# Optimization experiments

Measured on AMD Instinct MI355X. Metric: run time of the kernel, lower is better.

## Reference

```python
import jax, jax.numpy as jnp
import numpy as np

PART_BODY = jnp.array([4, 4, 0, 0, 1, 1, 2, 2, 3, 3], dtype=jnp.int32)  # joint -> body part
NUM_SUBSET = 3
BN_EPS = 1e-5
NEG_SLOPE = 0.1


def setup_inputs() -> dict:
    key = jax.random.key(0)
    ks = jax.random.split(key, 8)
    N, C, T, V, S = 32, 96, 1024, 10, NUM_SUBSET
    P = 5  # number of body parts
    return {
        "x": jax.random.normal(ks[0], (N, C, T, V), dtype=jnp.float32),
        "b_att": jax.random.normal(ks[1], (N, S, P, P), dtype=jnp.float32),
        "W_qkv": jax.random.normal(ks[2], (3 * C, C), dtype=jnp.float32) * (1.0 / np.sqrt(C)),
        "b_qkv": jax.random.normal(ks[3], (3 * C,), dtype=jnp.float32) * 0.01,
        "W_ff": jax.random.normal(ks[4], (C, C), dtype=jnp.float32) * (1.0 / np.sqrt(C)),
        "b_ff": jax.random.normal(ks[5], (C,), dtype=jnp.float32) * 0.01,
        "bn_gamma": jnp.ones((C,), dtype=jnp.float32),
        "bn_beta": jnp.zeros((C,), dtype=jnp.float32),
        "bn_mean": jnp.zeros((C,), dtype=jnp.float32),
        "bn_var": jnp.ones((C,), dtype=jnp.float32),
    }


def reference(x, b_att, W_qkv, b_qkv, W_ff, b_ff, bn_gamma, bn_beta, bn_mean, bn_var):
    N, C, T, V = x.shape
    S = NUM_SUBSET
    mid = C // S

    # 1x1 conv -> QKV: (N, 3C, T, V)
    qkv = jnp.einsum('nctv,oc->notv', x, W_qkv) + b_qkv[None, :, None, None]
    qkv = qkv.reshape(N, 3 * S, mid, T, V)
    q, k, v = jnp.split(qkv, 3, axis=1)  # each (N, S, mid, T, V)

    # joint-joint attention, contracted over channel and time
    attention0 = jnp.tanh(jnp.einsum('nsctu,nsctv->nsuv', q, k) / (mid * T))

    # gather body-part bias to joint resolution: (N, S, V, V)
    bb_att = b_att[:, :, PART_BODY[:, None], PART_BODY[None, :]]
    attention = attention0 + bb_att

    # apply attention to V
    y = jnp.einsum('nsuv,nsctv->nsctu', attention, v).reshape(N, C, T, V)

    # ff: 1x1 conv + BatchNorm (inference-style, running stats)
    y = jnp.einsum('nctv,oc->notv', y, W_ff) + b_ff[None, :, None, None]
    inv_std = (1.0 / jnp.sqrt(bn_var + BN_EPS))
    y = (y - bn_mean[None, :, None, None]) * (bn_gamma * inv_std)[None, :, None, None] + bn_beta[None, :, None, None]

    out = jax.nn.leaky_relu(x + y, negative_slope=NEG_SLOPE)
    return (out, attention0)
```

## Files before the change

### kernel.cpp

```cpp
#include <hip/hip_runtime.h>
#include <cstddef>

#define NN 32
#define CC 96
#define TT 1024
#define PP 10240
#define NEG 0.1f
#define GCH 8
#define MCH 4

typedef __attribute__((ext_vector_type(8))) short s16x8;
typedef __attribute__((ext_vector_type(4))) float f32x4;
typedef unsigned short ushort_t;
typedef unsigned int uint_t;
typedef unsigned long long ull_t;

#define OFF_ATT  ((size_t)NN*128*300)
#define OFF_WBF  (OFF_ATT + (size_t)NN*300)
#define OFF_WFB  (OFF_WBF + (size_t)13824)
#define OFF_BF   (OFF_WFB + (size_t)4608)

#define VP 82

__device__ __forceinline__ ushort_t f2bf(float f) {
    union { float f; uint_t u; } a; a.f = f;
    const uint_t r = a.u + 0x7FFFu + ((a.u >> 16) & 1u);
    return (ushort_t)(r >> 16);
}
__device__ __forceinline__ float bf2f(ushort_t h) {
    union { uint_t u; float f; } a; a.u = ((uint_t)h) << 16;
    return a.f;
}
__device__ __forceinline__ float tanh_inl(float z) {
    z = fminf(fmaxf(z, -10.f), 10.f);
    const float e2 = __expf(2.f * z);
    return (e2 - 1.f) / (e2 + 1.f);
}

__global__ void k_prep(const float* __restrict__ wqkv, const float* __restrict__ wff,
                       const float* __restrict__ bff,  const float* __restrict__ gam,
                       const float* __restrict__ bet,  const float* __restrict__ mu,
                       const float* __restrict__ var,  float* __restrict__ ws) {
    const int i = blockIdx.x * 256 + threadIdx.x;
    const int stride = gridDim.x * 256;
    ushort_t* wbf = (ushort_t*)(ws + OFF_WBF);
    for (int j = i; j < 288 * 96; j += stride) wbf[j] = f2bf(wqkv[j]);
    ushort_t* wfb = (ushort_t*)(ws + OFF_WFB);
    for (int j = i; j < 96 * 96; j += stride) {
        const int o = j / 96;
        const float A = gam[o] * rsqrtf(var[o] + 1e-5f);
        wfb[j] = f2bf(wff[j] * A);
    }
    for (int j = i; j < 96; j += stride) {
        const float A = gam[j] * rsqrtf(var[j] + 1e-5f);
        ws[OFF_BF + j] = (bff[j] - mu[j]) * A + bet[j];
    }
    for (int j = i; j < NN * 300; j += stride) ws[OFF_ATT + j] = 0.f;
}

__global__ __launch_bounds__(640) void k_gram(const float* __restrict__ x,
                                              const ushort_t* __restrict__ wbf,
                                              const float* __restrict__ bqkv,
                                              float* __restrict__ attsum) {
    __shared__ ushort_t xT[80][104];
    __shared__ ushort_t qk[6][8][10][36];
    __shared__ float red[6][100];
    const int n = blockIdx.y, tcb = blockIdx.x;
    const int tid = threadIdx.x;
    const int l = tid & 63, w = tid >> 6;
    const int lr = l & 15, lh = l >> 4;
    const int ct = w >> 1, rth = w & 1;
    const int p2p = ct * 16 + lr;

    int c4a[3], ppa[3];
#pragma unroll
    for (int it = 0; it < 3; it++) {
        const int i = tid + it * 640;
        c4a[it] = i / 80; ppa[it] = i % 80;
    }

    const float* xn = x + (size_t)n * CC * PP;
    float xr[12];
    {
        const float* xsrc = xn + (size_t)(tcb * GCH) * 80;
#pragma unroll
        for (int it = 0; it < 3; it++)
#pragma unroll
            for (int r = 0; r < 4; r++)
                xr[it * 4 + r] = xsrc[(size_t)(4 * c4a[it] + r) * PP + ppa[it]];
    }

    float gacc = 0.f;
    for (int j = 0; j < GCH; j++) {
#pragma unroll
        for (int it = 0; it < 3; it++) {
            const uint_t lo = (uint_t)f2bf(xr[it * 4 + 0]) | ((uint_t)f2bf(xr[it * 4 + 1]) << 16);
            const uint_t hi = (uint_t)f2bf(xr[it * 4 + 2]) | ((uint_t)f2bf(xr[it * 4 + 3]) << 16);
            *(ull_t*)&xT[ppa[it]][4 * c4a[it]] = (ull_t)lo | ((ull_t)hi << 32);
        }
        __syncthreads();

        if (j + 1 < GCH) {
            const float* xsrc = xn + (size_t)(tcb * GCH + j + 1) * 80;
#pragma unroll
            for (int it = 0; it < 3; it++)
#pragma unroll
                for (int r = 0; r < 4; r++)
                    xr[it * 4 + r] = xsrc[(size_t)(4 * c4a[it] + r) * PP + ppa[it]];
        }

        {
            s16x8 bfr[3];
#pragma unroll
            for (int kb = 0; kb < 3; kb++)
                bfr[kb] = *(const s16x8*)&xT[p2p][kb * 32 + lh * 8];
            ushort_t* qkf = (ushort_t*)qk;
#pragma unroll
            for (int jj = 0; jj < 6; jj++) {
                const int rt = rth * 6 + jj;
                f32x4 acc = {0.f, 0.f, 0.f, 0.f};
#pragma unroll
                for (int kb = 0; kb < 3; kb++) {
                    const s16x8 afr = *(const s16x8*)&wbf[(size_t)(rt * 16 + lr) * 96 + kb * 32 + lh * 8];
                    acc = __builtin_amdgcn_mfma_f32_16x16x32_bf16(afr, bfr[kb], acc, 0, 0, 0);
                }
                const int obase = rt * 16 + lh * 4;
                const float4 bb = *(const float4*)&bqkv[obase];
                const int role = rth;
                const int orem = obase - role * 96;
                const int s = orem >> 5, cp0 = orem & 31;
                const uint_t lo = (uint_t)f2bf(acc[0] + bb.x) | ((uint_t)f2bf(acc[1] + bb.y) << 16);
                const uint_t hi = (uint_t)f2bf(acc[2] + bb.z) | ((uint_t)f2bf(acc[3] + bb.w) << 16);
                *(ull_t*)(qkf + ((size_t)(role * 3 + s) * 80 + p2p) * 36 + cp0) =
                    (ull_t)lo | ((ull_t)hi << 32);
            }
        }
        __syncthreads();

        if (w < 6) {
            const int s = w >> 1, th = w & 1;
            const int uv = lr > 9 ? 9 : lr;
            f32x4 g = {0.f, 0.f, 0.f, 0.f};
#pragma unroll
            for (int t4 = 0; t4 < 4; t4++) {
                const int t = th * 4 + t4;
                const ushort_t* qp = &qk[s][t][uv][lh * 8];
                const ushort_t* kp = &qk[3 + s][t][uv][lh * 8];
                union { ull_t u[2]; s16x8 v; } ua, ub;
                ua.u[0] = *(const ull_t*)qp;  ua.u[1] = *(const ull_t*)(qp + 4);
                ub.u[0] = *(const ull_t*)kp;  ub.u[1] = *(const ull_t*)(kp + 4);
                g = __builtin_amdgcn_mfma_f32_16x16x32_bf16(ua.v, ub.v, g, 0, 0, 0);
            }
#pragma unroll
            for (int r = 0; r < 4; r++) {
                const int u = lh * 4 + r;
                if (u < 10 && lr < 10) red[w][u * 10 + lr] = g[r];
            }
        }
        __syncthreads();

        if (tid < 300) {
            const int s2 = tid / 100, r0 = tid % 100;
            gacc += red[s2 * 2][r0] + red[s2 * 2 + 1][r0];
        }
    }
    if (tid < 300) atomicAdd(&attsum[(size_t)n * 300 + tid], gacc);
}

__global__ __launch_bounds__(640) void k_mix(const float* __restrict__ x,
                                             const ushort_t* __restrict__ wbf,
                                             const float* __restrict__ bqkv,
                                             const float* __restrict__ attsum,
                                             const float* __restrict__ batt,
                                             const ushort_t* __restrict__ wfb,
                                             const float* __restrict__ bf,
                                             float* __restrict__ out,
                                             float* __restrict__ out_att0) {
    __shared__ ushort_t xT[80 * 104];
    __shared__ ushort_t vls[96 * VP];
    __shared__ float Als[304];
    const int n = blockIdx.y, tcb = blockIdx.x;
    const int tid = threadIdx.x;
    const int l = tid & 63, w = tid >> 6;
    const int lr = l & 15, lh = l >> 4;
    const int ct = w >> 1, rth = w & 1;
    const int plocal = ct * 16 + lr;

    if (tid < 300) {
        const float a0 = tanh_inl(attsum[(size_t)n * 300 + tid] * (1.0f / 32768.0f));
        if (tcb == 0) out_att0[(size_t)n * 300 + tid] = a0;
        const int s = tid / 100, r = tid % 100, u = r / 10, v = r % 10;
        const int pu = (u / 2 + 4) % 5, pv = (v / 2 + 4) % 5;
        Als[tid] = a0 + batt[((n * 3 + s) * 5 + pu) * 5 + pv];
    }

    int c4a[3], ppa[3];
#pragma unroll
    for (int it = 0; it < 3; it++) {
        const int i = tid + it * 640;
        c4a[it] = i / 80; ppa[it] = i % 80;
    }
    const int g8 = tid / 80;
    const int pcol = tid - g8 * 80;
    const int ucol = pcol % 10;
    const int tlb = pcol - ucol;

    const float* xn = x + (size_t)n * CC * PP;
    float xr[12];
    {
        const float* xsrc = xn + (size_t)(tcb * MCH) * 80;
#pragma unroll
        for (int it = 0; it < 3; it++)
#pragma unroll
            for (int r = 0; r < 4; r++)
                xr[it * 4 + r] = xsrc[(size_t)(4 * c4a[it] + r) * PP + ppa[it]];
    }

    for (int j = 0; j < MCH; j++) {
        const int tc80 = tcb * MCH + j;
#pragma unroll
        for (int it = 0; it < 3; it++) {
            const uint_t lo = (uint_t)f2bf(xr[it * 4 + 0]) | ((uint_t)f2bf(xr[it * 4 + 1]) << 16);
            const uint_t hi = (uint_t)f2bf(xr[it * 4 + 2]) | ((uint_t)f2bf(xr[it * 4 + 3]) << 16);
            *(ull_t*)&xT[ppa[it] * 104 + 4 * c4a[it]] = (ull_t)lo | ((ull_t)hi << 32);
        }
        __syncthreads();

        if (j + 1 < MCH) {
            const float* xsrc = xn + (size_t)(tc80 + 1) * 80;
#pragma unroll
            for (int it = 0; it < 3; it++)
#pragma unroll
                for (int r = 0; r < 4; r++)
                    xr[it * 4 + r] = xsrc[(size_t)(4 * c4a[it] + r) * PP + ppa[it]];
        }

        {
            s16x8 bfr[3];
#pragma unroll
            for (int kb = 0; kb < 3; kb++)
                bfr[kb] = *(const s16x8*)&xT[plocal * 104 + kb * 32 + lh * 8];
#pragma unroll
            for (int jj = 0; jj < 3; jj++) {
                const int rt = rth * 3 + jj;
                f32x4 acc = {0.f, 0.f, 0.f, 0.f};
#pragma unroll
                for (int kb = 0; kb < 3; kb++) {
                    const s16x8 afr = *(const s16x8*)&wbf[(size_t)(192 + rt * 16 + lr) * 96 + kb * 32 + lh * 8];
                    acc = __builtin_amdgcn_mfma_f32_16x16x32_bf16(afr, bfr[kb], acc, 0, 0, 0);
                }
                const int ob = 192 + rt * 16 + lh * 4;
                const float4 bb = *(const float4*)&bqkv[ob];
                const int o = rt * 16 + lh * 4;
                vls[(o + 0) * VP + plocal] = f2bf(acc[0] + bb.x);
                vls[(o + 1) * VP + plocal] = f2bf(acc[1] + bb.y);
                vls[(o + 2) * VP + plocal] = f2bf(acc[2] + bb.z);
                vls[(o + 3) * VP + plocal] = f2bf(acc[3] + bb.w);
            }
        }
        __syncthreads();

        {
            float aqk[10];
#pragma unroll
            for (int m = 0; m < 12; m++) {
                if ((m & 3) == 0) {
                    const int s = m >> 2;
#pragma unroll
                    for (int v = 0; v < 10; v++) aqk[v] = Als[s * 100 + ucol * 10 + v];
                }
                const int sc = m * 8 + g8;
                const ushort_t* vr = &vls[sc * VP + tlb];
                float y0 = 0.f;
#pragma unroll
                for (int h = 0; h < 5; h++) {
                    const uint_t two = *(const uint_t*)(vr + 2 * h);
                    union { uint_t uu; float ff; } lo, hi;
                    lo.uu = two << 16;
                    hi.uu = two & 0xFFFF0000u;
                    y0 = fmaf(aqk[2 * h],     lo.ff, y0);
                    y0 = fmaf(aqk[2 * h + 1], hi.ff, y0);
                }
                xT[pcol * 104 + sc] = f2bf(y0);
            }
        }
        __syncthreads();

        {
            s16x8 yfr[3];
#pragma unroll
            for (int kb = 0; kb < 3; kb++)
                yfr[kb] = *(const s16x8*)&xT[plocal * 104 + kb * 32 + lh * 8];
            const size_t pbase = (size_t)n * CC * PP + (size_t)tc80 * 80;
#pragma unroll
            for (int jj = 0; jj < 3; jj++) {
                const int rt = rth * 3 + jj;
                const int ob = rt * 16 + lh * 4;
                float xr4[4];
#pragma unroll
                for (int r = 0; r < 4; r++)
                    xr4[r] = x[pbase + (size_t)(ob + r) * PP + plocal];
                f32x4 acc = {0.f, 0.f, 0.f, 0.f};
#pragma unroll
                for (int kb = 0; kb < 3; kb++) {
                    const s16x8 faf = *(const s16x8*)&wfb[(size_t)(rt * 16 + lr) * 96 + kb * 32 + lh * 8];
                    acc = __builtin_amdgcn_mfma_f32_16x16x32_bf16(faf, yfr[kb], acc, 0, 0, 0);
                }
                const float4 bb = *(const float4*)&bf[ob];
#pragma unroll
                for (int r = 0; r < 4; r++) {
                    const size_t idx = pbase + (size_t)(ob + r) * PP + plocal;
                    const float rr = xr4[r] + acc[r] + ((const float*)&bb)[r];
                    out[idx] = rr > 0.f ? rr : NEG * rr;
                }
            }
        }
        __syncthreads();
    }
}

extern "C" void kernel_launch(void* const* d_in, const int* in_sizes, int n_in,
                              void* d_out, int out_size, void* d_ws, size_t ws_size,
                              hipStream_t stream) {
    const float* x    = (const float*)d_in[0];
    const float* batt = (const float*)d_in[1];
    const float* wqkv = (const float*)d_in[2];
    const float* bqkv = (const float*)d_in[3];
    const float* wff  = (const float*)d_in[4];
    const float* bff  = (const float*)d_in[5];
    const float* gam  = (const float*)d_in[6];
    const float* bet  = (const float*)d_in[7];
    const float* mu   = (const float*)d_in[8];
    const float* var  = (const float*)d_in[9];

    float* ws  = (float*)d_ws;
    float* out = (float*)d_out;
    float* out_att0 = out + (size_t)NN * CC * PP;

    float*    attsum = ws + OFF_ATT;
    ushort_t* wbf    = (ushort_t*)(ws + OFF_WBF);
    ushort_t* wfb    = (ushort_t*)(ws + OFF_WFB);
    float*    bfold  = ws + OFF_BF;

    hipLaunchKernelGGL(k_prep, dim3(64), dim3(256), 0, stream,
                       wqkv, wff, bff, gam, bet, mu, var, ws);
    hipLaunchKernelGGL(k_gram, dim3(128 / GCH, 32), dim3(640), 0, stream,
                       x, wbf, bqkv, attsum);
    hipLaunchKernelGGL(k_mix, dim3(128 / MCH, 32), dim3(640), 0, stream,
                       x, wbf, bqkv, attsum, batt, wfb, bfold, out, out_att0);
}
```

Measured before the change: 134.9 us.

## Separate y0 LDS buffer, vectorize attention-apply stores, drop a barrier per chunk

Adds a dedicated LDS buffer for the attention-applied values, so the x tile for the next chunk can be written into xT right after the final GEMM stage without waiting on an extra barrier. This removes one __syncthreads per chunk. The attention-apply stage is also remapped so each thread computes 8 consecutive channels and writes them as two 64-bit packed stores instead of scalar 16-bit stores. The cost is more LDS per block and a tail where only half the threads are active in the second pass.

```diff
diff --git a/kernel.cpp b/kernel.cpp
--- a/kernel.cpp
+++ b/kernel.cpp
@@ -178,6 +178,7 @@
                                              float* __restrict__ out_att0) {
     __shared__ ushort_t xT[80 * 104];
     __shared__ ushort_t vls[96 * VP];
+    __shared__ ushort_t y0T[80 * 104];
     __shared__ float Als[304];
     const int n = blockIdx.y, tcb = blockIdx.x;
     const int tid = threadIdx.x;
@@ -200,10 +201,10 @@
         const int i = tid + it * 640;
         c4a[it] = i / 80; ppa[it] = i % 80;
     }
-    const int g8 = tid / 80;
-    const int pcol = tid - g8 * 80;
-    const int ucol = pcol % 10;
-    const int tlb = pcol - ucol;
+    const int p4p  = tid % 80;
+    const int scb1 = tid / 80;
+    const int u4   = p4p % 10;
+    const int tlb4 = p4p - u4;
 
     const float* xn = x + (size_t)n * CC * PP;
     float xr[12];
@@ -214,17 +215,17 @@
 #pragma unroll
             for (int r = 0; r < 4; r++)
                 xr[it * 4 + r] = xsrc[(size_t)(4 * c4a[it] + r) * PP + ppa[it]];
-    }
-
-    for (int j = 0; j < MCH; j++) {
-        const int tc80 = tcb * MCH + j;
 #pragma unroll
         for (int it = 0; it < 3; it++) {
             const uint_t lo = (uint_t)f2bf(xr[it * 4 + 0]) | ((uint_t)f2bf(xr[it * 4 + 1]) << 16);
             const uint_t hi = (uint_t)f2bf(xr[it * 4 + 2]) | ((uint_t)f2bf(xr[it * 4 + 3]) << 16);
             *(ull_t*)&xT[ppa[it] * 104 + 4 * c4a[it]] = (ull_t)lo | ((ull_t)hi << 32);
         }
-        __syncthreads();
+    }
+    __syncthreads();
+
+    for (int j = 0; j < MCH; j++) {
+        const int tc80 = tcb * MCH + j;
 
         if (j + 1 < MCH) {
             const float* xsrc = xn + (size_t)(tc80 + 1) * 80;
@@ -260,28 +261,37 @@
         }
         __syncthreads();
 
-        {
-            float aqk[10];
-#pragma unroll
-            for (int m = 0; m < 12; m++) {
-                if ((m & 3) == 0) {
-                    const int s = m >> 2;
-#pragma unroll
-                    for (int v = 0; v < 10; v++) aqk[v] = Als[s * 100 + ucol * 10 + v];
-                }
-                const int sc = m * 8 + g8;
-                const ushort_t* vr = &vls[sc * VP + tlb];
-                float y0 = 0.f;
-#pragma unroll
-                for (int h = 0; h < 5; h++) {
-                    const uint_t two = *(const uint_t*)(vr + 2 * h);
-                    union { uint_t uu; float ff; } lo, hi;
-                    lo.uu = two << 16;
-                    hi.uu = two & 0xFFFF0000u;
-                    y0 = fmaf(aqk[2 * h],     lo.ff, y0);
-                    y0 = fmaf(aqk[2 * h + 1], hi.ff, y0);
-                }
-                xT[pcol * 104 + sc] = f2bf(y0);
+#pragma unroll
+        for (int half = 0; half < 2; half++) {
+            if (half == 0 || tid < 320) {
+                const int scb = scb1 + half * 8;
+                const int s = (half == 0) ? (scb1 >> 2) : 2;
+                float aqk[10];
+#pragma unroll
+                for (int v = 0; v < 10; v++) aqk[v] = Als[s * 100 + u4 * 10 + v];
+                float y0v[8];
+#pragma unroll
+                for (int e = 0; e < 8; e++) {
+                    const ushort_t* vr = &vls[(scb * 8 + e) * VP + tlb4];
+                    float y0 = 0.f;
+#pragma unroll
+                    for (int h = 0; h < 5; h++) {
+                        const uint_t two = *(const uint_t*)(vr + 2 * h);
+                        union { uint_t uu; float ff; } lo, hi;
+                        lo.uu = two << 16;
+                        hi.uu = two & 0xFFFF0000u;
+                        y0 = fmaf(aqk[2 * h],     lo.ff, y0);
+                        y0 = fmaf(aqk[2 * h + 1], hi.ff, y0);
+                    }
+                    y0v[e] = y0;
+                }
+                union { uint_t u[4]; ull_t q[2]; } pk;
+#pragma unroll
+                for (int e2 = 0; e2 < 4; e2++)
+                    pk.u[e2] = (uint_t)f2bf(y0v[2 * e2]) | ((uint_t)f2bf(y0v[2 * e2 + 1]) << 16);
+                ull_t* dst = (ull_t*)&y0T[p4p * 104 + scb * 8];
+                dst[0] = pk.q[0];
+                dst[1] = pk.q[1];
             }
         }
         __syncthreads();
@@ -290,7 +300,7 @@
             s16x8 yfr[3];
 #pragma unroll
             for (int kb = 0; kb < 3; kb++)
-                yfr[kb] = *(const s16x8*)&xT[plocal * 104 + kb * 32 + lh * 8];
+                yfr[kb] = *(const s16x8*)&y0T[plocal * 104 + kb * 32 + lh * 8];
             const size_t pbase = (size_t)n * CC * PP + (size_t)tc80 * 80;
 #pragma unroll
             for (int jj = 0; jj < 3; jj++) {
@@ -315,7 +325,15 @@
                 }
             }
         }
-        __syncthreads();
+        if (j + 1 < MCH) {
+#pragma unroll
+            for (int it = 0; it < 3; it++) {
+                const uint_t lo = (uint_t)f2bf(xr[it * 4 + 0]) | ((uint_t)f2bf(xr[it * 4 + 1]) << 16);
+                const uint_t hi = (uint_t)f2bf(xr[it * 4 + 2]) | ((uint_t)f2bf(xr[it * 4 + 3]) << 16);
+                *(ull_t*)&xT[ppa[it] * 104 + 4 * c4a[it]] = (ull_t)lo | ((ull_t)hi << 32);
+            }
+            __syncthreads();
+        }
     }
 }
 
```

Measured after the change: 145.6 us. 1.08x slower.
